# Kernel tuning notes

Hardware: AMD Instinct MI355X
Metric: run time of the kernel (lower is better)

## Reference

```python
import jax, jax.numpy as jnp
import numpy as np

DIM, HEADS, WS, MLP_RATIO = 384, 8, 8, 2.0
HID = int(DIM * MLP_RATIO)
EPS = 1e-5


def layernorm(x, w, b):
    mu = jnp.mean(x, axis=-1, keepdims=True)
    var = jnp.mean(jnp.square(x - mu), axis=-1, keepdims=True)
    return (x - mu) * jax.lax.rsqrt(var + EPS) * w + b


def setup_inputs() -> dict:
    key = jax.random.key(0)
    ks = jax.random.split(key, 8)
    s = 0.02
    return {
        "x": jax.random.normal(ks[0], (8, DIM, 128, 128), dtype=jnp.float32),
        "n1_w": jnp.ones((DIM,), jnp.float32),
        "n1_b": jnp.zeros((DIM,), jnp.float32),
        "in_w": jax.random.normal(ks[1], (3 * DIM, DIM), jnp.float32) * s,  # qkv packed, Linear convention
        "in_b": jnp.zeros((3 * DIM,), jnp.float32),
        "out_w": jax.random.normal(ks[2], (DIM, DIM), jnp.float32) * s,
        "out_b": jnp.zeros((DIM,), jnp.float32),
        "n2_w": jnp.ones((DIM,), jnp.float32),
        "n2_b": jnp.zeros((DIM,), jnp.float32),
        "w1": jax.random.normal(ks[3], (HID, DIM), jnp.float32) * s,
        "b1": jnp.zeros((HID,), jnp.float32),
        "w2": jax.random.normal(ks[4], (DIM, HID), jnp.float32) * s,
        "b2": jnp.zeros((DIM,), jnp.float32),
    }


def _block(x, n1_w, n1_b, in_w, in_b, out_w, out_b, n2_w, n2_b, w1, b1, w2, b2):
    b, c, h, w = x.shape
    ph = (WS - h % WS) % WS
    pw = (WS - w % WS) % WS
    if ph or pw:
        x = jnp.pad(x, ((0, 0), (0, 0), (0, ph), (0, pw)))
    hp, wp = x.shape[2], x.shape[3]
    nh, nw = hp // WS, wp // WS
    # window partition: [b,c,hp,wp] -> [b*nh*nw, WS*WS, c]
    win = x.reshape(b, c, nh, WS, nw, WS).transpose(0, 2, 4, 3, 5, 1).reshape(-1, WS * WS, c)

    y = layernorm(win, n1_w, n1_b)
    # packed qkv projection
    qkv = jnp.einsum('nsc,fc->nsf', y, in_w) + in_b  # [N, S, 3C]
    q, k, v = jnp.split(qkv, 3, axis=-1)
    hd = c // HEADS
    def split_heads(t):
        return t.reshape(t.shape[0], t.shape[1], HEADS, hd)
    q, k, v = split_heads(q), split_heads(k), split_heads(v)
    scale = 1.0 / np.sqrt(hd).astype(np.float32)
    att = jnp.einsum('nqhd,nkhd->nhqk', q * scale, k)
    att = jax.nn.softmax(att, axis=-1)
    o = jnp.einsum('nhqk,nkhd->nqhd', att, v).reshape(-1, WS * WS, c)
    o = jnp.einsum('nsc,fc->nsf', o, out_w) + out_b
    win = win + o

    y = layernorm(win, n2_w, n2_b)
    y = jax.nn.gelu(jnp.einsum('nsc,fc->nsf', y, w1) + b1, approximate=False)
    win = win + jnp.einsum('nsf,cf->nsc', y, w2) + b2

    # window reverse
    xo = win.reshape(b, nh, nw, WS, WS, c).transpose(0, 5, 1, 3, 2, 4).reshape(b, c, hp, wp)
    return xo[:, :, :h, :w]


def reference(x, n1_w, n1_b, in_w, in_b, out_w, out_b, n2_w, n2_b, w1, b1, w2, b2):
    return _block(x, n1_w, n1_b, in_w, in_b, out_w, out_b, n2_w, n2_b, w1, b1, w2, b2)
```

## Files before the change

### kernel.cpp

```cpp
#include <hip/hip_runtime.h>

#define NWIN 2048
#define TPB 256

typedef __attribute__((ext_vector_type(8))) short short8;
typedef __attribute__((ext_vector_type(4))) float floatx4;

__device__ __forceinline__ float bf2f(unsigned short u) {
    union { unsigned int i; float f; } v; v.i = ((unsigned int)u) << 16; return v.f;
}
__device__ __forceinline__ unsigned short f2bf(float f) {
    union { float f; unsigned int i; } v; v.f = f;
    unsigned int u = v.i;
    return (unsigned short)((u + 0x7FFFu + ((u >> 16) & 1u)) >> 16);
}
__device__ __forceinline__ floatx4 mfma16(short8 a, short8 b, floatx4 c) {
    return __builtin_amdgcn_mfma_f32_16x16x32_bf16(a, b, c, 0, 0, 0);
}

__global__ __launch_bounds__(TPB) void k0_cvt(
    const float* __restrict__ inw, const float* __restrict__ inb,
    const float* __restrict__ outw, const float* __restrict__ outb,
    const float* __restrict__ n1w, const float* __restrict__ n1b,
    const float* __restrict__ n2w, const float* __restrict__ n2b,
    const float* __restrict__ w1, const float* __restrict__ b1,
    const float* __restrict__ w2, const float* __restrict__ b2,
    unsigned short* __restrict__ dst)
{
    int i = blockIdx.x * TPB + threadIdx.x;
    if (i >= 1183872) return;
    const float* src; int off;
    if      (i < 442368)  { src = inw;  off = 0; }
    else if (i < 443520)  { src = inb;  off = 442368; }
    else if (i < 590976)  { src = outw; off = 443520; }
    else if (i < 591360)  { src = outb; off = 590976; }
    else if (i < 591744)  { src = n1w;  off = 591360; }
    else if (i < 592128)  { src = n1b;  off = 591744; }
    else if (i < 592512)  { src = n2w;  off = 592128; }
    else if (i < 592896)  { src = n2b;  off = 592512; }
    else if (i < 887808)  { src = w1;   off = 592896; }
    else if (i < 888576)  { src = b1;   off = 887808; }
    else if (i < 1183488) { src = w2;   off = 888576; }
    else                  { src = b2;   off = 1183488; }
    dst[i] = f2bf(src[i - off]);
}

__global__ __launch_bounds__(TPB) void k1_ln1(
    const float* __restrict__ x,
    const unsigned short* __restrict__ n1w,
    const unsigned short* __restrict__ n1b,
    unsigned short* __restrict__ ybuf)
{
    __shared__ __align__(16) unsigned short win[64][392];
    __shared__ float mu_s[64], rs_s[64];
    const int tid = threadIdx.x;
    const int widx = blockIdx.x;
    const int b = widx >> 8, nh = (widx >> 4) & 15, nw = widx & 15;
    const size_t xbase = (size_t)b * 384 * 16384 + (size_t)nh * 8 * 128 + (size_t)nw * 8;

    for (int idx = tid; idx < 6144; idx += TPB) {
        int c = idx >> 4, i = (idx >> 1) & 7, half = idx & 1;
        floatx4 v = *(const floatx4*)(x + xbase + (size_t)c * 16384 + i * 128 + half * 4);
        #pragma unroll
        for (int j = 0; j < 4; ++j) win[i * 8 + half * 4 + j][c] = f2bf(v[j]);
    }
    __syncthreads();
    {
        int row = tid >> 2, part = tid & 3;
        float s = 0.f, sq = 0.f;
        for (int c = part * 96; c < part * 96 + 96; ++c) {
            float f = bf2f(win[row][c]); s += f; sq += f * f;
        }
        s += __shfl_xor(s, 1); s += __shfl_xor(s, 2);
        sq += __shfl_xor(sq, 1); sq += __shfl_xor(sq, 2);
        float mu = s * (1.f / 384.f);
        float var = sq * (1.f / 384.f) - mu * mu;
        if (part == 0) { mu_s[row] = mu; rs_s[row] = rsqrtf(var + 1e-5f); }
    }
    __syncthreads();
    const size_t ybase = (size_t)widx * 24576;
    for (int idx = tid; idx < 3072; idx += TPB) {
        int r = idx / 48, c0 = (idx % 48) * 8;
        float mu = mu_s[r], rs = rs_s[r];
        short8 o;
        #pragma unroll
        for (int j = 0; j < 8; ++j) {
            int c = c0 + j;
            o[j] = (short)f2bf((bf2f(win[r][c]) - mu) * rs * bf2f(n1w[c]) + bf2f(n1b[c]));
        }
        *(short8*)(ybuf + ybase + idx * 8) = o;
    }
}

__global__ __launch_bounds__(512) void k2_attn(
    unsigned short* __restrict__ yo,
    const unsigned short* __restrict__ in_w,
    const unsigned short* __restrict__ in_b)
{
    __shared__ __align__(16) unsigned short ylds[24576];
    __shared__ __align__(16) unsigned short wbuf[8][6144];
    const int tid = threadIdx.x;
    const int h = tid >> 6, lane = tid & 63;
    const int l15 = lane & 15, lg = lane >> 4;
    const int widx = blockIdx.x;
    const size_t base = (size_t)widx * 24576;
    const short8 z8 = {0, 0, 0, 0, 0, 0, 0, 0};

    unsigned short* bufA = &wbuf[h][0];
    unsigned short* bufB = &wbuf[h][3072];

    for (int g = tid; g < 3072; g += 512) {
        int m = g / 48, kc = g % 48;
        short8 v = *(const short8*)(yo + base + g * 8);
        *(short8*)&ylds[m * 384 + ((kc ^ (m & 7)) << 3)] = v;
    }
    __syncthreads();

    const float scale = 0.14433756729740643f;
    const unsigned short* wq = in_w + (size_t)(h * 48) * 384;
    const unsigned short* wk = in_w + (size_t)(384 + h * 48) * 384;
    const unsigned short* wv = in_w + (size_t)(768 + h * 48) * 384;

    {
        floatx4 acc[4][6];
        #pragma unroll
        for (int mt = 0; mt < 4; ++mt)
            #pragma unroll
            for (int i = 0; i < 6; ++i) acc[mt][i] = (floatx4){0, 0, 0, 0};
        #pragma unroll 1
        for (int ks = 0; ks < 12; ++ks) {
            short8 a[4];
            #pragma unroll
            for (int mt = 0; mt < 4; ++mt) {
                int m = mt * 16 + l15;
                a[mt] = *(const short8*)&ylds[m * 384 + (((ks * 4 + lg) ^ (m & 7)) << 3)];
            }
            #pragma unroll
            for (int nt = 0; nt < 3; ++nt) {
                short8 bq = *(const short8*)(wq + (size_t)(nt * 16 + l15) * 384 + ks * 32 + lg * 8);
                #pragma unroll
                for (int mt = 0; mt < 4; ++mt) acc[mt][nt] = mfma16(a[mt], bq, acc[mt][nt]);
                short8 bk = *(const short8*)(wk + (size_t)(nt * 16 + l15) * 384 + ks * 32 + lg * 8);
                #pragma unroll
                for (int mt = 0; mt < 4; ++mt) acc[mt][3 + nt] = mfma16(a[mt], bk, acc[mt][3 + nt]);
            }
        }
        #pragma unroll
        for (int sel = 0; sel < 2; ++sel) {
            unsigned short* dst = sel ? bufB : bufA;
            #pragma unroll
            for (int nt = 0; nt < 3; ++nt) {
                int d = nt * 16 + l15;
                int g = d >> 3;
                float bias = bf2f(in_b[sel * 384 + h * 48 + d]);
                #pragma unroll
                for (int mt = 0; mt < 4; ++mt)
                    #pragma unroll
                    for (int r = 0; r < 4; ++r) {
                        int mm = mt * 16 + lg * 4 + r;
                        dst[mm * 48 + ((g ^ (mm & 1)) << 3) + (d & 7)] =
                            f2bf(acc[mt][sel * 3 + nt][r] + bias);
                    }
            }
        }
    }

    floatx4 sacc[4][4];
    #pragma unroll
    for (int mt = 0; mt < 4; ++mt)
        #pragma unroll
        for (int nt = 0; nt < 4; ++nt) sacc[mt][nt] = (floatx4){0, 0, 0, 0};
    {
        short8 b0[4], b1[4];
        #pragma unroll
        for (int nt = 0; nt < 4; ++nt) {
            int n = nt * 16 + l15;
            b0[nt] = *(const short8*)&bufB[n * 48 + ((lg ^ (n & 1)) << 3)];
            b1[nt] = (lg < 2) ? *(const short8*)&bufB[n * 48 + (((4 + lg) ^ (n & 1)) << 3)] : z8;
        }
        #pragma unroll
        for (int mt = 0; mt < 4; ++mt) {
            int mq = mt * 16 + l15;
            short8 a0 = *(const short8*)&bufA[mq * 48 + ((lg ^ (mq & 1)) << 3)];
            #pragma unroll
            for (int nt = 0; nt < 4; ++nt) sacc[mt][nt] = mfma16(a0, b0[nt], sacc[mt][nt]);
            short8 a1 = (lg < 2) ? *(const short8*)&bufA[mq * 48 + (((4 + lg) ^ (mq & 1)) << 3)] : z8;
            #pragma unroll
            for (int nt = 0; nt < 4; ++nt) sacc[mt][nt] = mfma16(a1, b1[nt], sacc[mt][nt]);
        }
    }

    #pragma unroll
    for (int mt = 0; mt < 4; ++mt)
        #pragma unroll
        for (int r = 0; r < 4; ++r) {
            float mx = fmaxf(fmaxf(sacc[mt][0][r], sacc[mt][1][r]),
                             fmaxf(sacc[mt][2][r], sacc[mt][3][r]));
            mx = fmaxf(mx, __shfl_xor(mx, 1));
            mx = fmaxf(mx, __shfl_xor(mx, 2));
            mx = fmaxf(mx, __shfl_xor(mx, 4));
            mx = fmaxf(mx, __shfl_xor(mx, 8));
            float e[4];
            #pragma unroll
            for (int nt = 0; nt < 4; ++nt) e[nt] = __expf(scale * (sacc[mt][nt][r] - mx));
            float sm = e[0] + e[1] + e[2] + e[3];
            sm += __shfl_xor(sm, 1); sm += __shfl_xor(sm, 2);
            sm += __shfl_xor(sm, 4); sm += __shfl_xor(sm, 8);
            float inv = 1.f / sm;
            #pragma unroll
            for (int nt = 0; nt < 4; ++nt) sacc[mt][nt][r] = e[nt] * inv;
        }

    #pragma unroll
    for (int mt = 0; mt < 4; ++mt)
        #pragma unroll
        for (int r = 0; r < 4; ++r) {
            int row = mt * 16 + lg * 4 + r;
            #pragma unroll
            for (int ntl = 0; ntl < 2; ++ntl) {
                int lc = ntl * 16 + l15;
                bufA[row * 32 + (((lc >> 3) ^ (row & 3)) << 3) + (lc & 7)] =
                    f2bf(sacc[mt][ntl][r]);
            }
        }

    floatx4 vacc[4][3];
    #pragma unroll
    for (int mt = 0; mt < 4; ++mt)
        #pragma unroll
        for (int nt = 0; nt < 3; ++nt) vacc[mt][nt] = (floatx4){0, 0, 0, 0};
    #pragma unroll 1
    for (int ks = 0; ks < 12; ++ks) {
        short8 a[4];
        #pragma unroll
        for (int mt = 0; mt < 4; ++mt) {
            int m = mt * 16 + l15;
            a[mt] = *(const short8*)&ylds[m * 384 + (((ks * 4 + lg) ^ (m & 7)) << 3)];
        }
        #pragma unroll
        for (int nt = 0; nt < 3; ++nt) {
            short8 bv = *(const short8*)(wv + (size_t)(nt * 16 + l15) * 384 + ks * 32 + lg * 8);
            #pragma unroll
            for (int mt = 0; mt < 4; ++mt) vacc[mt][nt] = mfma16(a[mt], bv, vacc[mt][nt]);
        }
    }
    #pragma unroll
    for (int nt = 0; nt < 3; ++nt) {
        int d = nt * 16 + l15;
        float bias = bf2f(in_b[768 + h * 48 + d]);
        #pragma unroll
        for (int mt = 0; mt < 4; ++mt)
            #pragma unroll
            for (int r = 0; r < 4; ++r) {
                int t = mt * 16 + lg * 4 + r;
                bufB[d * 64 + (((t >> 3) ^ (d & 7)) << 3) + (t & 7)] =
                    f2bf(vacc[mt][nt][r] + bias);
            }
    }

    floatx4 oacc[4][3];
    #pragma unroll
    for (int mt = 0; mt < 4; ++mt)
        #pragma unroll
        for (int nt = 0; nt < 3; ++nt) oacc[mt][nt] = (floatx4){0, 0, 0, 0};
    #pragma unroll
    for (int kh = 0; kh < 2; ++kh) {
        if (kh == 1) {
            #pragma unroll
            for (int mt = 0; mt < 4; ++mt)
                #pragma unroll
                for (int r = 0; r < 4; ++r) {
                    int row = mt * 16 + lg * 4 + r;
                    #pragma unroll
                    for (int ntl = 0; ntl < 2; ++ntl) {
                        int lc = ntl * 16 + l15;
                        bufA[row * 32 + (((lc >> 3) ^ (row & 3)) << 3) + (lc & 7)] =
                            f2bf(sacc[mt][2 + ntl][r]);
                    }
                }
        }
        #pragma unroll
        for (int mt = 0; mt < 4; ++mt) {
            int m = mt * 16 + l15;
            short8 a = *(const short8*)&bufA[m * 32 + ((lg ^ (m & 3)) << 3)];
            #pragma unroll
            for (int nt = 0; nt < 3; ++nt) {
                int d = nt * 16 + l15;
                int tg = kh * 4 + lg;
                short8 bb = *(const short8*)&bufB[d * 64 + ((tg ^ (d & 7)) << 3)];
                oacc[mt][nt] = mfma16(a, bb, oacc[mt][nt]);
            }
        }
    }
    #pragma unroll
    for (int nt = 0; nt < 3; ++nt)
        #pragma unroll
        for (int mt = 0; mt < 4; ++mt)
            #pragma unroll
            for (int r = 0; r < 4; ++r) {
                int mm = mt * 16 + lg * 4 + r;
                yo[base + (size_t)mm * 384 + h * 48 + nt * 16 + l15] = f2bf(oacc[mt][nt][r]);
            }
}

__global__ __launch_bounds__(TPB) void k3_proj(
    const float* __restrict__ x,
    unsigned short* __restrict__ ow,
    const unsigned short* __restrict__ out_w,
    const unsigned short* __restrict__ out_b)
{
    __shared__ __align__(16) unsigned short olds[24576];
    const int tid = threadIdx.x;
    const int wave = tid >> 6, lane = tid & 63;
    const int l15 = lane & 15, lg = lane >> 4;
    const int widx = blockIdx.x;
    const int b = widx >> 8, nh = (widx >> 4) & 15, nw = widx & 15;
    const size_t base = (size_t)widx * 24576;
    const size_t xbase = (size_t)b * 384 * 16384 + (size_t)nh * 8 * 128 + (size_t)nw * 8;

    for (int g = tid; g < 3072; g += TPB) {
        int m = g / 48, kc = g % 48;
        short8 v = *(const short8*)(ow + base + g * 8);
        *(short8*)&olds[m * 384 + ((kc ^ (m & 7)) << 3)] = v;
    }
    __syncthreads();

    floatx4 acc[24];
    #pragma unroll
    for (int i = 0; i < 24; ++i) acc[i] = (floatx4){0, 0, 0, 0};
    #pragma unroll 1
    for (int ks = 0; ks < 12; ++ks) {
        short8 a[4];
        #pragma unroll
        for (int mt = 0; mt < 4; ++mt) {
            int m = mt * 16 + l15;
            int kc = ks * 4 + lg;
            a[mt] = *(const short8*)&olds[m * 384 + ((kc ^ (m & 7)) << 3)];
        }
        #pragma unroll
        for (int nt = 0; nt < 6; ++nt) {
            int f = wave * 96 + nt * 16 + l15;
            short8 bb = *(const short8*)(out_w + (size_t)f * 384 + ks * 32 + lg * 8);
            #pragma unroll
            for (int mt = 0; mt < 4; ++mt)
                acc[nt * 4 + mt] = mfma16(a[mt], bb, acc[nt * 4 + mt]);
        }
    }
    #pragma unroll
    for (int nt = 0; nt < 6; ++nt) {
        int col = wave * 96 + nt * 16 + l15;
        float bias = bf2f(out_b[col]);
        #pragma unroll
        for (int mt = 0; mt < 4; ++mt) {
            #pragma unroll
            for (int r = 0; r < 4; ++r) {
                int m = mt * 16 + lg * 4 + r;
                int i = m >> 3, j = m & 7;
                float res = x[xbase + (size_t)col * 16384 + i * 128 + j];
                ow[base + (size_t)m * 384 + col] = f2bf(acc[nt * 4 + mt][r] + bias + res);
            }
        }
    }
}

__global__ __launch_bounds__(512) void k4_mlp(
    unsigned short* __restrict__ wbuf,
    const unsigned short* __restrict__ n2w,
    const unsigned short* __restrict__ n2b,
    const unsigned short* __restrict__ w1,
    const unsigned short* __restrict__ b1,
    const unsigned short* __restrict__ w2,
    const unsigned short* __restrict__ b2)
{
    __shared__ __align__(16) unsigned short ylds[64][392];
    __shared__ __align__(16) unsigned short hlds[64][776];
    const int tid = threadIdx.x;
    const int wave = tid >> 6, lane = tid & 63;
    const int l15 = lane & 15, lg = lane >> 4;
    const int widx = blockIdx.x;
    const size_t base = (size_t)widx * 24576;

    {
        int row = tid >> 3, part = tid & 7;
        const unsigned short* src = wbuf + base + row * 384 + part * 48;
        float s = 0.f, sq = 0.f;
        #pragma unroll
        for (int g = 0; g < 6; ++g) {
            short8 v = *(const short8*)(src + g * 8);
            #pragma unroll
            for (int j = 0; j < 8; ++j) { float f = bf2f((unsigned short)v[j]); s += f; sq += f * f; }
        }
        s += __shfl_xor(s, 1); s += __shfl_xor(s, 2); s += __shfl_xor(s, 4);
        sq += __shfl_xor(sq, 1); sq += __shfl_xor(sq, 2); sq += __shfl_xor(sq, 4);
        float mu = s * (1.f / 384.f);
        float rs = rsqrtf(sq * (1.f / 384.f) - mu * mu + 1e-5f);
        #pragma unroll
        for (int g = 0; g < 6; ++g) {
            short8 v = *(const short8*)(src + g * 8);
            short8 o;
            #pragma unroll
            for (int j = 0; j < 8; ++j) {
                int c = part * 48 + g * 8 + j;
                o[j] = (short)f2bf((bf2f((unsigned short)v[j]) - mu) * rs * bf2f(n2w[c]) + bf2f(n2b[c]));
            }
            *(short8*)&ylds[row][part * 48 + g * 8] = o;
        }
    }
    __syncthreads();

    {
        floatx4 acc[24];
        #pragma unroll
        for (int i = 0; i < 24; ++i) acc[i] = (floatx4){0, 0, 0, 0};
        #pragma unroll 1
        for (int ks = 0; ks < 12; ++ks) {
            short8 a[4];
            #pragma unroll
            for (int mt = 0; mt < 4; ++mt)
                a[mt] = *(const short8*)&ylds[mt * 16 + l15][ks * 32 + lg * 8];
            #pragma unroll
            for (int nt = 0; nt < 6; ++nt) {
                int f = wave * 96 + nt * 16 + l15;
                short8 bb = *(const short8*)(w1 + (size_t)f * 384 + ks * 32 + lg * 8);
                #pragma unroll
                for (int mt = 0; mt < 4; ++mt)
                    acc[nt * 4 + mt] = mfma16(a[mt], bb, acc[nt * 4 + mt]);
            }
        }
        #pragma unroll
        for (int nt = 0; nt < 6; ++nt) {
            int col = wave * 96 + nt * 16 + l15;
            float bias = bf2f(b1[col]);
            #pragma unroll
            for (int mt = 0; mt < 4; ++mt) {
                #pragma unroll
                for (int r = 0; r < 4; ++r) {
                    float v = acc[nt * 4 + mt][r] + bias;
                    float g = 0.5f * v * (1.f + erff(v * 0.70710678118654752f));
                    hlds[mt * 16 + lg * 4 + r][col] = f2bf(g);
                }
            }
        }
    }
    __syncthreads();

    {
        floatx4 acc2[12];
        #pragma unroll
        for (int i = 0; i < 12; ++i) acc2[i] = (floatx4){0, 0, 0, 0};
        #pragma unroll 1
        for (int ks = 0; ks < 24; ++ks) {
            short8 a[4];
            #pragma unroll
            for (int mt = 0; mt < 4; ++mt)
                a[mt] = *(const short8*)&hlds[mt * 16 + l15][ks * 32 + lg * 8];
            #pragma unroll
            for (int nt = 0; nt < 3; ++nt) {
                int c = wave * 48 + nt * 16 + l15;
                short8 bb = *(const short8*)(w2 + (size_t)c * 768 + ks * 32 + lg * 8);
                #pragma unroll
                for (int mt = 0; mt < 4; ++mt)
                    acc2[nt * 4 + mt] = mfma16(a[mt], bb, acc2[nt * 4 + mt]);
            }
        }
        #pragma unroll
        for (int nt = 0; nt < 3; ++nt) {
            int col = wave * 48 + nt * 16 + l15;
            float bias = bf2f(b2[col]);
            #pragma unroll
            for (int mt = 0; mt < 4; ++mt) {
                #pragma unroll
                for (int r = 0; r < 4; ++r) {
                    int mm = mt * 16 + lg * 4 + r;
                    float res = bf2f(wbuf[base + (size_t)mm * 384 + col]);
                    wbuf[base + (size_t)mm * 384 + col] = f2bf(acc2[nt * 4 + mt][r] + bias + res);
                }
            }
        }
    }
}

__global__ __launch_bounds__(TPB) void k5_out(
    const unsigned short* __restrict__ res,
    float* __restrict__ out)
{
    __shared__ __align__(16) unsigned short t[128][200];
    const int tid = threadIdx.x;
    const int bid = blockIdx.x;
    const int ch = bid & 1, i = (bid >> 1) & 7, nh = (bid >> 4) & 15, b = bid >> 8;

    {
        int wrow = tid >> 1, half = tid & 1;
        int nw = wrow >> 3, j = wrow & 7;
        size_t rbase = (size_t)(((b * 16 + nh) * 16) + nw) * 24576 + (i * 8 + j) * 384 + ch * 192;
        #pragma unroll
        for (int g = 0; g < 12; ++g) {
            int cc = half * 12 + g;
            short8 v = *(const short8*)(res + rbase + cc * 8);
            *(short8*)&t[wrow][cc * 8] = v;
        }
    }
    __syncthreads();
    {
        int q = tid >> 5, wg = tid & 31;
        int w0 = wg * 4;
        size_t obase = ((size_t)b * 384 + ch * 192) * 16384 + (size_t)(nh * 8 + i) * 128 + w0;
        #pragma unroll 1
        for (int cc = 0; cc < 24; ++cc) {
            int cp = cc * 8 + q;
            floatx4 v;
            #pragma unroll
            for (int k = 0; k < 4; ++k) v[k] = bf2f(t[w0 + k][cp]);
            *(floatx4*)(out + obase + (size_t)cp * 16384) = v;
        }
    }
}

extern "C" void kernel_launch(void* const* d_in, const int* in_sizes, int n_in,
                              void* d_out, int out_size, void* d_ws, size_t ws_size,
                              hipStream_t stream) {
    (void)in_sizes; (void)n_in; (void)out_size; (void)ws_size;
    const float* x    = (const float*)d_in[0];
    const float* n1w  = (const float*)d_in[1];
    const float* n1b  = (const float*)d_in[2];
    const float* inw  = (const float*)d_in[3];
    const float* inb  = (const float*)d_in[4];
    const float* outw = (const float*)d_in[5];
    const float* outb = (const float*)d_in[6];
    const float* n2w  = (const float*)d_in[7];
    const float* n2b  = (const float*)d_in[8];
    const float* w1   = (const float*)d_in[9];
    const float* b1   = (const float*)d_in[10];
    const float* w2   = (const float*)d_in[11];
    const float* b2   = (const float*)d_in[12];
    unsigned short* wsu  = (unsigned short*)d_ws;
    unsigned short* ybuf = wsu;
    unsigned short* wb   = wsu + 50331648;
    const unsigned short* inw_b  = wb;
    const unsigned short* inb_b  = wb + 442368;
    const unsigned short* outw_b = wb + 443520;
    const unsigned short* outb_b = wb + 590976;
    const unsigned short* n1w_b  = wb + 591360;
    const unsigned short* n1b_b  = wb + 591744;
    const unsigned short* n2w_b  = wb + 592128;
    const unsigned short* n2b_b  = wb + 592512;
    const unsigned short* w1_b   = wb + 592896;
    const unsigned short* b1_b   = wb + 887808;
    const unsigned short* w2_b   = wb + 888576;
    const unsigned short* b2_b   = wb + 1183488;
    float* out = (float*)d_out;

    k0_cvt<<<dim3((1183872 + TPB - 1) / TPB), dim3(TPB), 0, stream>>>(
        inw, inb, outw, outb, n1w, n1b, n2w, n2b, w1, b1, w2, b2, wb);
    k1_ln1<<<dim3(NWIN), dim3(TPB), 0, stream>>>(x, n1w_b, n1b_b, ybuf);
    k2_attn<<<dim3(NWIN), dim3(512), 0, stream>>>(ybuf, inw_b, inb_b);
    k3_proj<<<dim3(NWIN), dim3(TPB), 0, stream>>>(x, ybuf, outw_b, outb_b);
    k4_mlp<<<dim3(NWIN), dim3(512), 0, stream>>>(ybuf, n2w_b, n2b_b, w1_b, b1_b, w2_b, b2_b);
    k5_out<<<dim3(NWIN), dim3(TPB), 0, stream>>>(ybuf, out);
}
```

Before: 1.423 ms.

## Fuse LN1 and output projection into attention kernel; chunk MLP hidden dim

Merges the LN1 kernel and the out-projection kernel into the attention kernel. The window is loaded from x straight into a swizzled LDS tile, normalized in place, and each head's output is kept in LDS so the out-projection and residual add run in the same block. This removes two launches and the global round-trips of the LN1 output and the attention output. The MLP kernel now processes the hidden dimension in three chunks of 256 with a smaller swizzled LDS buffer and launch_bounds(512,4), aiming for higher occupancy at the cost of extra barriers.

```diff
diff --git a/kernel.cpp b/kernel.cpp
--- a/kernel.cpp
+++ b/kernel.cpp
@@ -45,57 +45,15 @@
     dst[i] = f2bf(src[i - off]);
 }
 
-__global__ __launch_bounds__(TPB) void k1_ln1(
+__global__ __launch_bounds__(512) void k2_attn(
     const float* __restrict__ x,
+    unsigned short* __restrict__ yo,
     const unsigned short* __restrict__ n1w,
     const unsigned short* __restrict__ n1b,
-    unsigned short* __restrict__ ybuf)
-{
-    __shared__ __align__(16) unsigned short win[64][392];
-    __shared__ float mu_s[64], rs_s[64];
-    const int tid = threadIdx.x;
-    const int widx = blockIdx.x;
-    const int b = widx >> 8, nh = (widx >> 4) & 15, nw = widx & 15;
-    const size_t xbase = (size_t)b * 384 * 16384 + (size_t)nh * 8 * 128 + (size_t)nw * 8;
-
-    for (int idx = tid; idx < 6144; idx += TPB) {
-        int c = idx >> 4, i = (idx >> 1) & 7, half = idx & 1;
-        floatx4 v = *(const floatx4*)(x + xbase + (size_t)c * 16384 + i * 128 + half * 4);
-        #pragma unroll
-        for (int j = 0; j < 4; ++j) win[i * 8 + half * 4 + j][c] = f2bf(v[j]);
-    }
-    __syncthreads();
-    {
-        int row = tid >> 2, part = tid & 3;
-        float s = 0.f, sq = 0.f;
-        for (int c = part * 96; c < part * 96 + 96; ++c) {
-            float f = bf2f(win[row][c]); s += f; sq += f * f;
-        }
-        s += __shfl_xor(s, 1); s += __shfl_xor(s, 2);
-        sq += __shfl_xor(sq, 1); sq += __shfl_xor(sq, 2);
-        float mu = s * (1.f / 384.f);
-        float var = sq * (1.f / 384.f) - mu * mu;
-        if (part == 0) { mu_s[row] = mu; rs_s[row] = rsqrtf(var + 1e-5f); }
-    }
-    __syncthreads();
-    const size_t ybase = (size_t)widx * 24576;
-    for (int idx = tid; idx < 3072; idx += TPB) {
-        int r = idx / 48, c0 = (idx % 48) * 8;
-        float mu = mu_s[r], rs = rs_s[r];
-        short8 o;
-        #pragma unroll
-        for (int j = 0; j < 8; ++j) {
-            int c = c0 + j;
-            o[j] = (short)f2bf((bf2f(win[r][c]) - mu) * rs * bf2f(n1w[c]) + bf2f(n1b[c]));
-        }
-        *(short8*)(ybuf + ybase + idx * 8) = o;
-    }
-}
-
-__global__ __launch_bounds__(512) void k2_attn(
-    unsigned short* __restrict__ yo,
     const unsigned short* __restrict__ in_w,
-    const unsigned short* __restrict__ in_b)
+    const unsigned short* __restrict__ in_b,
+    const unsigned short* __restrict__ out_w,
+    const unsigned short* __restrict__ out_b)
 {
     __shared__ __align__(16) unsigned short ylds[24576];
     __shared__ __align__(16) unsigned short wbuf[8][6144];
@@ -103,16 +61,53 @@
     const int h = tid >> 6, lane = tid & 63;
     const int l15 = lane & 15, lg = lane >> 4;
     const int widx = blockIdx.x;
+    const int b = widx >> 8, nh = (widx >> 4) & 15, nw = widx & 15;
     const size_t base = (size_t)widx * 24576;
+    const size_t xbase = (size_t)b * 384 * 16384 + (size_t)nh * 8 * 128 + (size_t)nw * 8;
     const short8 z8 = {0, 0, 0, 0, 0, 0, 0, 0};
 
     unsigned short* bufA = &wbuf[h][0];
     unsigned short* bufB = &wbuf[h][3072];
 
-    for (int g = tid; g < 3072; g += 512) {
-        int m = g / 48, kc = g % 48;
-        short8 v = *(const short8*)(yo + base + g * 8);
-        *(short8*)&ylds[m * 384 + ((kc ^ (m & 7)) << 3)] = v;
+    for (int idx = tid; idx < 6144; idx += 512) {
+        int c = idx >> 4, i = (idx >> 1) & 7, half = idx & 1;
+        floatx4 v = *(const floatx4*)(x + xbase + (size_t)c * 16384 + i * 128 + half * 4);
+        #pragma unroll
+        for (int j = 0; j < 4; ++j) {
+            int m = i * 8 + half * 4 + j;
+            ylds[m * 384 + (((c >> 3) ^ (m & 7)) << 3) + (c & 7)] = f2bf(v[j]);
+        }
+    }
+    __syncthreads();
+
+    {
+        int row = tid >> 3, part = tid & 7;
+        float s = 0.f, sq = 0.f;
+        #pragma unroll
+        for (int g = 0; g < 6; ++g) {
+            int ck = part * 6 + g;
+            short8 v = *(const short8*)&ylds[row * 384 + ((ck ^ (row & 7)) << 3)];
+            #pragma unroll
+            for (int j = 0; j < 8; ++j) { float f = bf2f((unsigned short)v[j]); s += f; sq += f * f; }
+        }
+        s += __shfl_xor(s, 1); s += __shfl_xor(s, 2); s += __shfl_xor(s, 4);
+        sq += __shfl_xor(sq, 1); sq += __shfl_xor(sq, 2); sq += __shfl_xor(sq, 4);
+        float mu = s * (1.f / 384.f);
+        float rs = rsqrtf(sq * (1.f / 384.f) - mu * mu + 1e-5f);
+        #pragma unroll
+        for (int g = 0; g < 6; ++g) {
+            int ck = part * 6 + g;
+            unsigned short* p = &ylds[row * 384 + ((ck ^ (row & 7)) << 3)];
+            short8 v = *(const short8*)p;
+            short8 wv = *(const short8*)(n1w + ck * 8);
+            short8 bv = *(const short8*)(n1b + ck * 8);
+            short8 o;
+            #pragma unroll
+            for (int j = 0; j < 8; ++j)
+                o[j] = (short)f2bf((bf2f((unsigned short)v[j]) - mu) * rs *
+                                   bf2f((unsigned short)wv[j]) + bf2f((unsigned short)bv[j]));
+            *(short8*)p = o;
+        }
     }
     __syncthreads();
 
@@ -299,71 +294,57 @@
             #pragma unroll
             for (int r = 0; r < 4; ++r) {
                 int mm = mt * 16 + lg * 4 + r;
-                yo[base + (size_t)mm * 384 + h * 48 + nt * 16 + l15] = f2bf(oacc[mt][nt][r]);
-            }
-}
-
-__global__ __launch_bounds__(TPB) void k3_proj(
-    const float* __restrict__ x,
-    unsigned short* __restrict__ ow,
-    const unsigned short* __restrict__ out_w,
-    const unsigned short* __restrict__ out_b)
-{
-    __shared__ __align__(16) unsigned short olds[24576];
-    const int tid = threadIdx.x;
-    const int wave = tid >> 6, lane = tid & 63;
-    const int l15 = lane & 15, lg = lane >> 4;
-    const int widx = blockIdx.x;
-    const int b = widx >> 8, nh = (widx >> 4) & 15, nw = widx & 15;
-    const size_t base = (size_t)widx * 24576;
-    const size_t xbase = (size_t)b * 384 * 16384 + (size_t)nh * 8 * 128 + (size_t)nw * 8;
-
-    for (int g = tid; g < 3072; g += TPB) {
-        int m = g / 48, kc = g % 48;
-        short8 v = *(const short8*)(ow + base + g * 8);
-        *(short8*)&olds[m * 384 + ((kc ^ (m & 7)) << 3)] = v;
-    }
+                int d = nt * 16 + l15;
+                bufA[mm * 48 + (((d >> 3) ^ (mm & 1)) << 3) + (d & 7)] =
+                    f2bf(oacc[mt][nt][r]);
+            }
     __syncthreads();
 
-    floatx4 acc[24];
-    #pragma unroll
-    for (int i = 0; i < 24; ++i) acc[i] = (floatx4){0, 0, 0, 0};
-    #pragma unroll 1
-    for (int ks = 0; ks < 12; ++ks) {
-        short8 a[4];
-        #pragma unroll
-        for (int mt = 0; mt < 4; ++mt) {
-            int m = mt * 16 + l15;
-            int kc = ks * 4 + lg;
-            a[mt] = *(const short8*)&olds[m * 384 + ((kc ^ (m & 7)) << 3)];
-        }
-        #pragma unroll
-        for (int nt = 0; nt < 6; ++nt) {
-            int f = wave * 96 + nt * 16 + l15;
-            short8 bb = *(const short8*)(out_w + (size_t)f * 384 + ks * 32 + lg * 8);
-            #pragma unroll
-            for (int mt = 0; mt < 4; ++mt)
-                acc[nt * 4 + mt] = mfma16(a[mt], bb, acc[nt * 4 + mt]);
-        }
-    }
-    #pragma unroll
-    for (int nt = 0; nt < 6; ++nt) {
-        int col = wave * 96 + nt * 16 + l15;
-        float bias = bf2f(out_b[col]);
-        #pragma unroll
-        for (int mt = 0; mt < 4; ++mt) {
-            #pragma unroll
-            for (int r = 0; r < 4; ++r) {
-                int m = mt * 16 + lg * 4 + r;
-                int i = m >> 3, j = m & 7;
-                float res = x[xbase + (size_t)col * 16384 + i * 128 + j];
-                ow[base + (size_t)m * 384 + col] = f2bf(acc[nt * 4 + mt][r] + bias + res);
-            }
-        }
-    }
-}
-
-__global__ __launch_bounds__(512) void k4_mlp(
+    {
+        floatx4 acc[3][4];
+        #pragma unroll
+        for (int nt = 0; nt < 3; ++nt)
+            #pragma unroll
+            for (int mt = 0; mt < 4; ++mt) acc[nt][mt] = (floatx4){0, 0, 0, 0};
+        #pragma unroll 1
+        for (int ks = 0; ks < 12; ++ks) {
+            int col8 = ks * 4 + lg;
+            int hh = (col8 * 43) >> 8;
+            int lc = col8 - hh * 6;
+            short8 a[4];
+            #pragma unroll
+            for (int mt = 0; mt < 4; ++mt) {
+                int m = mt * 16 + l15;
+                a[mt] = *(const short8*)&wbuf[hh][m * 48 + ((lc ^ (m & 1)) << 3)];
+            }
+            #pragma unroll
+            for (int nt = 0; nt < 3; ++nt) {
+                int f = h * 48 + nt * 16 + l15;
+                short8 bb = *(const short8*)(out_w + (size_t)f * 384 + ks * 32 + lg * 8);
+                #pragma unroll
+                for (int mt = 0; mt < 4; ++mt)
+                    acc[nt][mt] = mfma16(a[mt], bb, acc[nt][mt]);
+            }
+        }
+        #pragma unroll
+        for (int nt = 0; nt < 3; ++nt) {
+            int col = h * 48 + nt * 16 + l15;
+            float bias = bf2f(out_b[col]);
+            #pragma unroll
+            for (int mt = 0; mt < 4; ++mt) {
+                #pragma unroll
+                for (int r = 0; r < 4; ++r) {
+                    int m = mt * 16 + lg * 4 + r;
+                    int i = m >> 3, j = m & 7;
+                    float res = x[xbase + (size_t)col * 16384 + i * 128 + j];
+                    yo[base + (size_t)m * 384 + col] = f2bf(acc[nt][mt][r] + bias + res);
+                }
+            }
+        }
+    }
+}
+
+__global__ __launch_bounds__(512, 4) void k4_mlp(
     unsigned short* __restrict__ wbuf,
     const unsigned short* __restrict__ n2w,
     const unsigned short* __restrict__ n2b,
@@ -372,8 +353,8 @@
     const unsigned short* __restrict__ w2,
     const unsigned short* __restrict__ b2)
 {
-    __shared__ __align__(16) unsigned short ylds[64][392];
-    __shared__ __align__(16) unsigned short hlds[64][776];
+    __shared__ __align__(16) unsigned short ylds[24576];
+    __shared__ __align__(16) unsigned short hch[16384];
     const int tid = threadIdx.x;
     const int wave = tid >> 6, lane = tid & 63;
     const int l15 = lane & 15, lg = lane >> 4;
@@ -396,31 +377,40 @@
         float rs = rsqrtf(sq * (1.f / 384.f) - mu * mu + 1e-5f);
         #pragma unroll
         for (int g = 0; g < 6; ++g) {
+            int ck = part * 6 + g;
             short8 v = *(const short8*)(src + g * 8);
+            short8 wv = *(const short8*)(n2w + ck * 8);
+            short8 bv = *(const short8*)(n2b + ck * 8);
             short8 o;
             #pragma unroll
-            for (int j = 0; j < 8; ++j) {
-                int c = part * 48 + g * 8 + j;
-                o[j] = (short)f2bf((bf2f((unsigned short)v[j]) - mu) * rs * bf2f(n2w[c]) + bf2f(n2b[c]));
-            }
-            *(short8*)&ylds[row][part * 48 + g * 8] = o;
+            for (int j = 0; j < 8; ++j)
+                o[j] = (short)f2bf((bf2f((unsigned short)v[j]) - mu) * rs *
+                                   bf2f((unsigned short)wv[j]) + bf2f((unsigned short)bv[j]));
+            *(short8*)&ylds[row * 384 + ((ck ^ (row & 7)) << 3)] = o;
         }
     }
     __syncthreads();
 
-    {
-        floatx4 acc[24];
-        #pragma unroll
-        for (int i = 0; i < 24; ++i) acc[i] = (floatx4){0, 0, 0, 0};
+    floatx4 acc2[12];
+    #pragma unroll
+    for (int i = 0; i < 12; ++i) acc2[i] = (floatx4){0, 0, 0, 0};
+
+    #pragma unroll 1
+    for (int cc = 0; cc < 3; ++cc) {
+        floatx4 acc[8];
+        #pragma unroll
+        for (int i = 0; i < 8; ++i) acc[i] = (floatx4){0, 0, 0, 0};
         #pragma unroll 1
         for (int ks = 0; ks < 12; ++ks) {
             short8 a[4];
             #pragma unroll
-            for (int mt = 0; mt < 4; ++mt)
-                a[mt] = *(const short8*)&ylds[mt * 16 + l15][ks * 32 + lg * 8];
-            #pragma unroll
-            for (int nt = 0; nt < 6; ++nt) {
-                int f = wave * 96 + nt * 16 + l15;
+            for (int mt = 0; mt < 4; ++mt) {
+                int m = mt * 16 + l15;
+                a[mt] = *(const short8*)&ylds[m * 384 + (((ks * 4 + lg) ^ (m & 7)) << 3)];
+            }
+            #pragma unroll
+            for (int nt = 0; nt < 2; ++nt) {
+                int f = cc * 256 + wave * 32 + nt * 16 + l15;
                 short8 bb = *(const short8*)(w1 + (size_t)f * 384 + ks * 32 + lg * 8);
                 #pragma unroll
                 for (int mt = 0; mt < 4; ++mt)
@@ -428,53 +418,52 @@
             }
         }
         #pragma unroll
-        for (int nt = 0; nt < 6; ++nt) {
-            int col = wave * 96 + nt * 16 + l15;
-            float bias = bf2f(b1[col]);
+        for (int nt = 0; nt < 2; ++nt) {
+            int dloc = wave * 32 + nt * 16 + l15;
+            float bias = bf2f(b1[cc * 256 + dloc]);
             #pragma unroll
             for (int mt = 0; mt < 4; ++mt) {
                 #pragma unroll
                 for (int r = 0; r < 4; ++r) {
+                    int t = mt * 16 + lg * 4 + r;
                     float v = acc[nt * 4 + mt][r] + bias;
                     float g = 0.5f * v * (1.f + erff(v * 0.70710678118654752f));
-                    hlds[mt * 16 + lg * 4 + r][col] = f2bf(g);
+                    hch[t * 256 + (((dloc >> 3) ^ (t & 7)) << 3) + (dloc & 7)] = f2bf(g);
                 }
             }
         }
-    }
-    __syncthreads();
-
-    {
-        floatx4 acc2[12];
-        #pragma unroll
-        for (int i = 0; i < 12; ++i) acc2[i] = (floatx4){0, 0, 0, 0};
+        __syncthreads();
         #pragma unroll 1
-        for (int ks = 0; ks < 24; ++ks) {
+        for (int ks = 0; ks < 8; ++ks) {
             short8 a[4];
             #pragma unroll
-            for (int mt = 0; mt < 4; ++mt)
-                a[mt] = *(const short8*)&hlds[mt * 16 + l15][ks * 32 + lg * 8];
+            for (int mt = 0; mt < 4; ++mt) {
+                int m = mt * 16 + l15;
+                a[mt] = *(const short8*)&hch[m * 256 + (((ks * 4 + lg) ^ (m & 7)) << 3)];
+            }
             #pragma unroll
             for (int nt = 0; nt < 3; ++nt) {
                 int c = wave * 48 + nt * 16 + l15;
-                short8 bb = *(const short8*)(w2 + (size_t)c * 768 + ks * 32 + lg * 8);
+                short8 bb = *(const short8*)(w2 + (size_t)c * 768 + cc * 256 + ks * 32 + lg * 8);
                 #pragma unroll
                 for (int mt = 0; mt < 4; ++mt)
                     acc2[nt * 4 + mt] = mfma16(a[mt], bb, acc2[nt * 4 + mt]);
             }
         }
-        #pragma unroll
-        for (int nt = 0; nt < 3; ++nt) {
-            int col = wave * 48 + nt * 16 + l15;
-            float bias = bf2f(b2[col]);
-            #pragma unroll
-            for (int mt = 0; mt < 4; ++mt) {
-                #pragma unroll
-                for (int r = 0; r < 4; ++r) {
-                    int mm = mt * 16 + lg * 4 + r;
-                    float res = bf2f(wbuf[base + (size_t)mm * 384 + col]);
-                    wbuf[base + (size_t)mm * 384 + col] = f2bf(acc2[nt * 4 + mt][r] + bias + res);
-                }
+        __syncthreads();
+    }
+
+    #pragma unroll
+    for (int nt = 0; nt < 3; ++nt) {
+        int col = wave * 48 + nt * 16 + l15;
+        float bias = bf2f(b2[col]);
+        #pragma unroll
+        for (int mt = 0; mt < 4; ++mt) {
+            #pragma unroll
+            for (int r = 0; r < 4; ++r) {
+                int mm = mt * 16 + lg * 4 + r;
+                float res = bf2f(wbuf[base + (size_t)mm * 384 + col]);
+                wbuf[base + (size_t)mm * 384 + col] = f2bf(acc2[nt * 4 + mt][r] + bias + res);
             }
         }
     }
@@ -552,9 +541,8 @@
 
     k0_cvt<<<dim3((1183872 + TPB - 1) / TPB), dim3(TPB), 0, stream>>>(
         inw, inb, outw, outb, n1w, n1b, n2w, n2b, w1, b1, w2, b2, wb);
-    k1_ln1<<<dim3(NWIN), dim3(TPB), 0, stream>>>(x, n1w_b, n1b_b, ybuf);
-    k2_attn<<<dim3(NWIN), dim3(512), 0, stream>>>(ybuf, inw_b, inb_b);
-    k3_proj<<<dim3(NWIN), dim3(TPB), 0, stream>>>(x, ybuf, outw_b, outb_b);
+    k2_attn<<<dim3(NWIN), dim3(512), 0, stream>>>(
+        x, ybuf, n1w_b, n1b_b, inw_b, inb_b, outw_b, outb_b);
     k4_mlp<<<dim3(NWIN), dim3(512), 0, stream>>>(ybuf, n2w_b, n2b_b, w1_b, b1_b, w2_b, b2_b);
     k5_out<<<dim3(NWIN), dim3(TPB), 0, stream>>>(ybuf, out);
 }
```

Result: faster. 1.323 ms (-7.0%).
